# Performance work log

Measured on AMD Instinct MI355X. Metric: run time of the kernel, lower is better.

Reference implementation:

```python
import jax, jax.numpy as jnp
import numpy as np

B, T, D, O, E = 4, 4096, 256, 256, 16


def setup_inputs() -> dict:
    key = jax.random.key(0)
    ks = jax.random.split(key, 5)
    s_in = 1.0 / np.sqrt(D)
    x = jax.random.normal(ks[0], (B, T, D), dtype=jnp.float32)
    We = jax.random.uniform(ks[1], (E, D, O), minval=-s_in, maxval=s_in, dtype=jnp.float32)
    be = jax.random.uniform(ks[2], (E, O), minval=-s_in, maxval=s_in, dtype=jnp.float32)
    Wg = jax.random.uniform(ks[3], (D, E), minval=-s_in, maxval=s_in, dtype=jnp.float32)
    bg = jax.random.uniform(ks[4], (E,), minval=-s_in, maxval=s_in, dtype=jnp.float32)
    return {"x": x, "We": We, "be": be, "Wg": Wg, "bg": bg}


def reference(x, We, be, Wg, bg):
    # gate: softmax over experts  [B,T,E]
    gate = jax.nn.softmax(jnp.einsum("btd,de->bte", x, Wg) + bg, axis=-1)
    # all experts: batched GEMM  [B,T,E,O]
    h = jax.nn.gelu(jnp.einsum("btd,edo->bteo", x, We) + be, approximate=False)
    # softmax-weighted sum over experts  [B,T,O]
    return jnp.einsum("bteo,bte->bto", h, gate)
```

## Files before the change

### kernel.cpp

```cpp
#include <hip/hip_runtime.h>
#include <stdint.h>

#define KD 256
#define NO 256
#define NE 16
#define BM 64
#define BN 128
#define XROW 264
#define NFRAG 128

typedef short bf16x8 __attribute__((ext_vector_type(8)));
typedef float f32x4 __attribute__((ext_vector_type(4)));

__device__ __forceinline__ unsigned short f2bf(float f) {
  uint32_t u = __float_as_uint(f);
  u += 0x7fffu + ((u >> 16) & 1u);
  return (unsigned short)(u >> 16);
}
__device__ __forceinline__ float bf2f(unsigned short h) {
  return __uint_as_float(((uint32_t)h) << 16);
}
__device__ __forceinline__ float gelu_f(float h) {
  float z = h * fmaf(0.07135481627f, h * h, 1.5957691216f);
  return h * __builtin_amdgcn_rcpf(1.0f + __expf(-z));
}

__global__ void moe_prep(const float* __restrict__ We, unsigned short* __restrict__ Wf,
                         const float* __restrict__ Wg, unsigned short* __restrict__ Wgt)
{
  __shared__ float ts[256 * 17];
  const int tid = threadIdx.x;
  const int bid = blockIdx.x;
  if (bid < 256) {
    const int e = bid >> 4, ob = bid & 15;
    const float* src = We + (size_t)e * KD * NO + ob * 16;
    const int o = tid & 15, dg = tid >> 4;
#pragma unroll
    for (int p = 0; p < 16; ++p) {
      int d = p * 16 + dg;
      ts[d * 17 + o] = src[(size_t)d * NO + o];
    }
    __syncthreads();
    const int w = tid >> 6, l = tid & 63;
    const int q = l >> 4, ln = l & 15;
#pragma unroll
    for (int kk = 0; kk < 2; ++kk) {
      int kc = w + kk * 4;
      unsigned int pk[4];
#pragma unroll
      for (int h = 0; h < 4; ++h) {
        unsigned short lo = f2bf(ts[(kc * 32 + q * 8 + h * 2 + 0) * 17 + ln]);
        unsigned short hi = f2bf(ts[(kc * 32 + q * 8 + h * 2 + 1) * 17 + ln]);
        pk[h] = (unsigned int)lo | ((unsigned int)hi << 16);
      }
      uint4* dst = (uint4*)(Wf + ((((size_t)(e * 8 + kc) * 16 + ob) * 64) + l) * 8);
      *dst = make_uint4(pk[0], pk[1], pk[2], pk[3]);
    }
  } else {
    int d = tid;
    const float* wr = Wg + (size_t)d * NE;
#pragma unroll
    for (int e = 0; e < NE; ++e)
      Wgt[e * KD + d] = f2bf(wr[e]);
  }
}

__launch_bounds__(256, 2)
__global__ void moe_main(const float* __restrict__ x,
                         const uint4* __restrict__ Wf,
                         const unsigned short* __restrict__ Wgt,
                         const float* __restrict__ be,
                         const float* __restrict__ bg,
                         float* __restrict__ out)
{
  __shared__ __align__(16) unsigned short Xs[BM * XROW];
  __shared__ float gate_t[NE * 65];
  __shared__ unsigned short be_h[NE * BN];

  const int tid = threadIdx.x;
  const int bid = blockIdx.x;
  const int half = bid & 1;
  const int n0 = half * BN;
  const int m0 = (bid >> 1) * BM;
  const int wid = tid >> 6, lane = tid & 63;
  const int wm = wid >> 1, wn = wid & 1;
  const int ln = lane & 15, quad = lane >> 4;

  const int voff = (half * 8 + wn * 4) * 64 + lane;

  {
    const float4* xg = (const float4*)x + (size_t)m0 * (KD / 4);
#pragma unroll
    for (int p = 0; p < 16; ++p) {
      int idx = p * 256 + tid;
      int r = idx >> 6, c = idx & 63;
      float4 v = xg[r * (KD / 4) + c];
      uint32_t lo = (uint32_t)f2bf(v.x) | ((uint32_t)f2bf(v.y) << 16);
      uint32_t hi = (uint32_t)f2bf(v.z) | ((uint32_t)f2bf(v.w) << 16);
      *(uint2*)&Xs[r * XROW + c * 4] = make_uint2(lo, hi);
    }
  }
#pragma unroll
  for (int p = 0; p < 8; ++p) {
    int idx = p * 256 + tid;
    int e = idx >> 7, c = idx & 127;
    be_h[e * BN + c] = f2bf(be[e * NO + n0 + c]);
  }
  __syncthreads();

  bf16x8 a[2][8];
  const int arow = wm * 32 + ln;
#pragma unroll
  for (int i = 0; i < 2; ++i)
#pragma unroll
    for (int kc = 0; kc < 8; ++kc)
      a[i][kc] = *(const bf16x8*)&Xs[(arow + i * 16) * XROW + kc * 32 + quad * 8];

  uint4 b[4][4];
#pragma unroll
  for (int t = 0; t < 4; ++t) {
    const uint4* p = Wf + (size_t)t * 1024 + voff;
    b[t][0] = p[0]; b[t][1] = p[64]; b[t][2] = p[128]; b[t][3] = p[192];
  }

  {
    f32x4 g0 = {0.f, 0.f, 0.f, 0.f}, g1 = {0.f, 0.f, 0.f, 0.f};
#pragma unroll
    for (int kc = 0; kc < 8; ++kc) {
      bf16x8 wb = *(const bf16x8*)(Wgt + (size_t)ln * KD + kc * 32 + quad * 8);
      g0 = __builtin_amdgcn_mfma_f32_16x16x32_bf16(a[0][kc], wb, g0, 0, 0, 0);
      g1 = __builtin_amdgcn_mfma_f32_16x16x32_bf16(a[1][kc], wb, g1, 0, 0, 0);
    }
    float bgl = bg[ln];
#pragma unroll
    for (int i = 0; i < 2; ++i)
#pragma unroll
      for (int r = 0; r < 4; ++r) {
        float v = (i == 0 ? g0[r] : g1[r]) + bgl;
        float mx = v;
#pragma unroll
        for (int msk = 1; msk < 16; msk <<= 1)
          mx = fmaxf(mx, __shfl_xor(mx, msk, 64));
        float ev = __expf(v - mx);
        float s = ev;
#pragma unroll
        for (int msk = 1; msk < 16; msk <<= 1)
          s += __shfl_xor(s, msk, 64);
        float gv = ev * __builtin_amdgcn_rcpf(s);
        if (wn == 0)
          gate_t[ln * 65 + wm * 32 + i * 16 + quad * 4 + r] = gv;
      }
  }
  __syncthreads();

  f32x4 acc[2][4], oacc[2][4];
#pragma unroll
  for (int i = 0; i < 2; ++i)
#pragma unroll
    for (int j = 0; j < 4; ++j) {
      acc[i][j] = (f32x4){0.f, 0.f, 0.f, 0.f};
      oacc[i][j] = (f32x4){0.f, 0.f, 0.f, 0.f};
    }

#pragma unroll 1
  for (int e = 0; e < NE; ++e) {
#pragma unroll
    for (int h = 0; h < 4; ++h) {
      const int t = e * 8 + h * 2;
#pragma unroll
      for (int s = 0; s < 2; ++s) {
        const int kc = h * 2 + s;
        uint4* bc = b[(t + s) & 3];
#pragma unroll
        for (int i = 0; i < 2; ++i)
#pragma unroll
          for (int j = 0; j < 4; ++j)
            acc[i][j] = __builtin_amdgcn_mfma_f32_16x16x32_bf16(
                a[i][kc], *(const bf16x8*)&bc[j], acc[i][j], 0, 0, 0);
        if (t + s + 4 < NFRAG) {
          const uint4* p = Wf + (size_t)(t + s + 4) * 1024 + voff;
          bc[0] = p[0]; bc[1] = p[64]; bc[2] = p[128]; bc[3] = p[192];
        }
      }
    }
    {
      const int brow = wn * 64 + ln;
      float gv[2][4];
#pragma unroll
      for (int i = 0; i < 2; ++i)
#pragma unroll
        for (int r = 0; r < 4; ++r)
          gv[i][r] = gate_t[e * 65 + wm * 32 + i * 16 + quad * 4 + r];
#pragma unroll
      for (int j = 0; j < 4; ++j) {
        float bias = bf2f(be_h[e * BN + brow + j * 16]);
#pragma unroll
        for (int i = 0; i < 2; ++i)
#pragma unroll
          for (int r = 0; r < 4; ++r) {
            float hh = acc[i][j][r] + bias;
            oacc[i][j][r] = fmaf(gv[i][r], gelu_f(hh), oacc[i][j][r]);
            acc[i][j][r] = 0.f;
          }
      }
    }
  }

#pragma unroll
  for (int i = 0; i < 2; ++i)
#pragma unroll
    for (int r = 0; r < 4; ++r) {
      int row = m0 + wm * 32 + i * 16 + quad * 4 + r;
      float* orow = out + (size_t)row * NO + n0 + wn * 64 + ln;
      orow[0]  = oacc[i][0][r];
      orow[16] = oacc[i][1][r];
      orow[32] = oacc[i][2][r];
      orow[48] = oacc[i][3][r];
    }
}

extern "C" void kernel_launch(void* const* d_in, const int* in_sizes, int n_in,
                              void* d_out, int out_size, void* d_ws, size_t ws_size,
                              hipStream_t stream) {
  const float* x  = (const float*)d_in[0];
  const float* We = (const float*)d_in[1];
  const float* be = (const float*)d_in[2];
  const float* Wg = (const float*)d_in[3];
  const float* bg = (const float*)d_in[4];
  float* out = (float*)d_out;
  unsigned short* Wf  = (unsigned short*)d_ws;
  unsigned short* Wgt = (unsigned short*)((char*)d_ws + (size_t)NE * NO * KD * 2);

  moe_prep<<<257, 256, 0, stream>>>(We, Wf, Wg, Wgt);
  moe_main<<<512, 256, 0, stream>>>(x, (const uint4*)Wf, Wgt, be, bg, out);
}
```

Baseline: 127.7 us.

## Remap warp tiling so each wave covers all 64 rows and 32 columns

```diff
diff --git a/kernel.cpp b/kernel.cpp
--- a/kernel.cpp
+++ b/kernel.cpp
@@ -82,11 +82,10 @@
   const int half = bid & 1;
   const int n0 = half * BN;
   const int m0 = (bid >> 1) * BM;
-  const int wid = tid >> 6, lane = tid & 63;
-  const int wm = wid >> 1, wn = wid & 1;
+  const int w = tid >> 6, lane = tid & 63;
   const int ln = lane & 15, quad = lane >> 4;
 
-  const int voff = (half * 8 + wn * 4) * 64 + lane;
+  const int voff = (half * 8 + w * 2) * 64 + lane;
 
   {
     const float4* xg = (const float4*)x + (size_t)m0 * (KD / 4);
@@ -108,114 +107,104 @@
   }
   __syncthreads();
 
-  bf16x8 a[2][8];
-  const int arow = wm * 32 + ln;
-#pragma unroll
-  for (int i = 0; i < 2; ++i)
+  bf16x8 a[4][8];
+#pragma unroll
+  for (int i = 0; i < 4; ++i)
 #pragma unroll
     for (int kc = 0; kc < 8; ++kc)
-      a[i][kc] = *(const bf16x8*)&Xs[(arow + i * 16) * XROW + kc * 32 + quad * 8];
-
-  uint4 b[4][4];
+      a[i][kc] = *(const bf16x8*)&Xs[(i * 16 + ln) * XROW + kc * 32 + quad * 8];
+
+  uint4 b[4][2];
 #pragma unroll
   for (int t = 0; t < 4; ++t) {
-    const uint4* p = Wf + (size_t)t * 1024 + voff;
-    b[t][0] = p[0]; b[t][1] = p[64]; b[t][2] = p[128]; b[t][3] = p[192];
+    const uint4* p = Wf + t * 1024 + voff;
+    b[t][0] = p[0]; b[t][1] = p[64];
   }
 
   {
-    f32x4 g0 = {0.f, 0.f, 0.f, 0.f}, g1 = {0.f, 0.f, 0.f, 0.f};
+    f32x4 g = {0.f, 0.f, 0.f, 0.f};
 #pragma unroll
     for (int kc = 0; kc < 8; ++kc) {
+      bf16x8 af = *(const bf16x8*)&Xs[(w * 16 + ln) * XROW + kc * 32 + quad * 8];
       bf16x8 wb = *(const bf16x8*)(Wgt + (size_t)ln * KD + kc * 32 + quad * 8);
-      g0 = __builtin_amdgcn_mfma_f32_16x16x32_bf16(a[0][kc], wb, g0, 0, 0, 0);
-      g1 = __builtin_amdgcn_mfma_f32_16x16x32_bf16(a[1][kc], wb, g1, 0, 0, 0);
+      g = __builtin_amdgcn_mfma_f32_16x16x32_bf16(af, wb, g, 0, 0, 0);
     }
     float bgl = bg[ln];
 #pragma unroll
-    for (int i = 0; i < 2; ++i)
-#pragma unroll
-      for (int r = 0; r < 4; ++r) {
-        float v = (i == 0 ? g0[r] : g1[r]) + bgl;
-        float mx = v;
-#pragma unroll
-        for (int msk = 1; msk < 16; msk <<= 1)
-          mx = fmaxf(mx, __shfl_xor(mx, msk, 64));
-        float ev = __expf(v - mx);
-        float s = ev;
-#pragma unroll
-        for (int msk = 1; msk < 16; msk <<= 1)
-          s += __shfl_xor(s, msk, 64);
-        float gv = ev * __builtin_amdgcn_rcpf(s);
-        if (wn == 0)
-          gate_t[ln * 65 + wm * 32 + i * 16 + quad * 4 + r] = gv;
-      }
+    for (int r = 0; r < 4; ++r) {
+      float v = g[r] + bgl;
+      float mx = v;
+#pragma unroll
+      for (int msk = 1; msk < 16; msk <<= 1)
+        mx = fmaxf(mx, __shfl_xor(mx, msk, 64));
+      float ev = __expf(v - mx);
+      float s = ev;
+#pragma unroll
+      for (int msk = 1; msk < 16; msk <<= 1)
+        s += __shfl_xor(s, msk, 64);
+      gate_t[ln * 65 + w * 16 + quad * 4 + r] = ev * __builtin_amdgcn_rcpf(s);
+    }
   }
   __syncthreads();
 
-  f32x4 acc[2][4], oacc[2][4];
-#pragma unroll
-  for (int i = 0; i < 2; ++i)
-#pragma unroll
-    for (int j = 0; j < 4; ++j) {
+  f32x4 acc[4][2], oacc[4][2];
+#pragma unroll
+  for (int i = 0; i < 4; ++i)
+#pragma unroll
+    for (int j = 0; j < 2; ++j) {
       acc[i][j] = (f32x4){0.f, 0.f, 0.f, 0.f};
       oacc[i][j] = (f32x4){0.f, 0.f, 0.f, 0.f};
     }
 
+  const uint4* pw = Wf + 4 * 1024 + voff;
+
 #pragma unroll 1
   for (int e = 0; e < NE; ++e) {
 #pragma unroll
-    for (int h = 0; h < 4; ++h) {
-      const int t = e * 8 + h * 2;
-#pragma unroll
-      for (int s = 0; s < 2; ++s) {
-        const int kc = h * 2 + s;
-        uint4* bc = b[(t + s) & 3];
-#pragma unroll
-        for (int i = 0; i < 2; ++i)
-#pragma unroll
-          for (int j = 0; j < 4; ++j)
-            acc[i][j] = __builtin_amdgcn_mfma_f32_16x16x32_bf16(
-                a[i][kc], *(const bf16x8*)&bc[j], acc[i][j], 0, 0, 0);
-        if (t + s + 4 < NFRAG) {
-          const uint4* p = Wf + (size_t)(t + s + 4) * 1024 + voff;
-          bc[0] = p[0]; bc[1] = p[64]; bc[2] = p[128]; bc[3] = p[192];
-        }
+    for (int kc = 0; kc < 8; ++kc) {
+      const int t = e * 8 + kc;
+      uint4* bc = b[t & 3];
+#pragma unroll
+      for (int i = 0; i < 4; ++i)
+#pragma unroll
+        for (int j = 0; j < 2; ++j)
+          acc[i][j] = __builtin_amdgcn_mfma_f32_16x16x32_bf16(
+              a[i][kc], *(const bf16x8*)&bc[j], acc[i][j], 0, 0, 0);
+      if (t + 4 < NFRAG) {
+        bc[0] = pw[0]; bc[1] = pw[64];
+        pw += 1024;
       }
     }
     {
-      const int brow = wn * 64 + ln;
-      float gv[2][4];
-#pragma unroll
-      for (int i = 0; i < 2; ++i)
+      float gv[4][4];
+#pragma unroll
+      for (int i = 0; i < 4; ++i)
 #pragma unroll
         for (int r = 0; r < 4; ++r)
-          gv[i][r] = gate_t[e * 65 + wm * 32 + i * 16 + quad * 4 + r];
-#pragma unroll
-      for (int j = 0; j < 4; ++j) {
-        float bias = bf2f(be_h[e * BN + brow + j * 16]);
-#pragma unroll
-        for (int i = 0; i < 2; ++i)
+          gv[i][r] = gate_t[e * 65 + i * 16 + quad * 4 + r];
+      float bb0 = bf2f(be_h[e * BN + w * 32 + ln]);
+      float bb1 = bf2f(be_h[e * BN + w * 32 + 16 + ln]);
+#pragma unroll
+      for (int i = 0; i < 4; ++i)
+#pragma unroll
+        for (int j = 0; j < 2; ++j)
 #pragma unroll
           for (int r = 0; r < 4; ++r) {
-            float hh = acc[i][j][r] + bias;
+            float hh = acc[i][j][r] + (j ? bb1 : bb0);
             oacc[i][j][r] = fmaf(gv[i][r], gelu_f(hh), oacc[i][j][r]);
             acc[i][j][r] = 0.f;
           }
-      }
-    }
-  }
-
-#pragma unroll
-  for (int i = 0; i < 2; ++i)
+    }
+  }
+
+#pragma unroll
+  for (int i = 0; i < 4; ++i)
 #pragma unroll
     for (int r = 0; r < 4; ++r) {
-      int row = m0 + wm * 32 + i * 16 + quad * 4 + r;
-      float* orow = out + (size_t)row * NO + n0 + wn * 64 + ln;
+      int row = m0 + i * 16 + quad * 4 + r;
+      float* orow = out + (size_t)row * NO + n0 + w * 32 + ln;
       orow[0]  = oacc[i][0][r];
       orow[16] = oacc[i][1][r];
-      orow[32] = oacc[i][2][r];
-      orow[48] = oacc[i][3][r];
     }
 }
 
```

After: 123.1 us. 3.6% less time.
